# Kernel tuning notes

Measured on AMD Instinct MI355X. Metric: run time of the kernel, lower is better.

The kernel has to match this reference:

```python
import jax, jax.numpy as jnp
import numpy as np

ALPHA = 1.0          # temperature of the Bayesian DP (init kwarg alpha)
NEG = -1e9           # -inf surrogate, safe in fp32/bf16


def conv1d_same(x, w, b):
    # x: [B, T, Cin], w: [K, Cin, Cout], 'SAME' padding, stride 1
    y = jax.lax.conv_general_dilated(x, w, window_strides=(1,), padding='SAME',
                                     dimension_numbers=('NWC', 'WIO', 'NWC'))
    return y + b


def postnet(x, ws, bs):
    # Tacotron-style conv PostNet: n_conv conv1d layers with tanh (dropout=0, eval mode)
    for w, b in zip(ws, bs):
        x = jnp.tanh(conv1d_same(x, w, b))
    return x


def bayesian_dp(W, alpha):
    """Monotonic-alignment Bayesian DP (Gumbel propagation).

    W: [B, T, S] node weights on the alignment grid (T = mel time, S = text).
    Each node (t, s) has two parents: (t-1, s) [stay] and (t-1, s-1) [advance].
      mu[t,s] = W[t,s] + (1/alpha) * logsumexp(alpha*mu[t-1,s], alpha*mu[t-1,s-1])
      pi[t,s] = softmax over the two parents -> [B, T, S, 2]
    """
    B, T, S = W.shape
    m0 = W[:, 0] + jnp.where(jnp.arange(S) == 0, 0.0, NEG)   # path must start at (0,0)
    pi0 = jnp.broadcast_to(jnp.array([1.0, 0.0], W.dtype), (B, S, 2))

    def step(prev, w_t):
        # prev: [B, S] = mu[t-1]; shifted: mu[t-1, s-1]
        shifted = jnp.concatenate([jnp.full((B, 1), NEG, prev.dtype), prev[:, :-1]], axis=1)
        stacked = jnp.stack([prev, shifted], axis=-1)         # [B, S, 2]
        m = w_t + jax.nn.logsumexp(alpha * stacked, axis=-1) / alpha
        pi_t = jax.nn.softmax(alpha * stacked, axis=-1)
        return m, (m, pi_t)

    _, (ms, pis) = jax.lax.scan(step, m0, jnp.swapaxes(W, 0, 1)[1:])  # scan over T-1
    mu = jnp.concatenate([m0[:, None], jnp.swapaxes(ms, 0, 1)], axis=1)    # [B, T, S]
    pi = jnp.concatenate([pi0[:, None], jnp.swapaxes(pis, 0, 1)], axis=1)  # [B, T, S, 2]
    return mu, pi


def setup_inputs() -> dict:
    key = jax.random.key(0)
    ks = jax.random.split(key, 6)
    B, T, S = 32, 2000, 400
    NMELS, H, K = 80, 256, 5
    inputs = jax.random.normal(ks[0], (B, T, NMELS), dtype=jnp.float32)
    src_enc = jax.random.normal(ks[1], (B, S, H), dtype=jnp.float32)
    mask = jnp.ones((B, T, S), dtype=jnp.float32)
    w1 = jax.random.normal(ks[2], (K, NMELS, H), dtype=jnp.float32) * 0.05
    w2 = jax.random.normal(ks[3], (K, H, H), dtype=jnp.float32) * 0.05
    w3 = jax.random.normal(ks[4], (K, H, H), dtype=jnp.float32) * 0.05
    b1 = jnp.zeros((H,), jnp.float32)
    b2 = jnp.zeros((H,), jnp.float32)
    b3 = jnp.zeros((H,), jnp.float32)
    return {"inputs": inputs, "src_enc": src_enc, "mask": mask,
            "w1": w1, "b1": b1, "w2": w2, "b2": b2, "w3": w3, "b3": b3}


def reference(inputs, src_enc, mask, w1, b1, w2, b2, w3, b3):
    # PostNet over mel frames -> spec embeddings matching src_enc dim
    Wspec = postnet(inputs, [w1, w2, w3], [b1, b2, b3])       # [B, T, H]
    # attention score grid
    W = jnp.einsum('bth,bsh->bts', Wspec, src_enc)            # [B, T, S]
    alignments = jax.nn.softmax(W, axis=1)                    # softmax over mel-time (dim 1)
    mu, pi = bayesian_dp(alignments * mask, ALPHA)
    return mu, pi, alignments, Wspec
```

## Files before the change

kernel.cpp:

```cpp
#include <hip/hip_runtime.h>
#include <hip/hip_bf16.h>

#define B_ 32
#define T_ 2000
#define S_ 400
#define C0_ 80
#define H_ 256

static constexpr float NEGV = -1e9f;
static constexpr int NMU  = B_ * T_ * S_;
static constexpr int NPI  = 2 * NMU;

typedef _Float16 f16x8 __attribute__((ext_vector_type(8)));
typedef float    f32x4 __attribute__((ext_vector_type(4)));

__global__ __launch_bounds__(256)
void wprep(const float* __restrict__ w, _Float16* __restrict__ wcat,
           int CIN, int CPAD)
{
  const int tot = 256 * 5 * CPAD;
  int idx = blockIdx.x * 256 + threadIdx.x;
  if (idx >= tot) return;
  int co  = idx / (5 * CPAD);
  int rem = idx - co * (5 * CPAD);
  int k   = rem / CPAD;
  int ci  = rem - k * CPAD;
  float v = (ci < CIN) ? w[((size_t)k * CIN + ci) * H_ + co] : 0.f;
  wcat[idx] = (_Float16)v;
}

__global__ __launch_bounds__(256)
void ecast(const float* __restrict__ e, _Float16* __restrict__ ef)
{
  const int n4 = B_ * S_ * H_ / 4;
  int idx = blockIdx.x * 256 + threadIdx.x;
  if (idx >= n4) return;
  float4 v = ((const float4*)e)[idx];
  _Float16* d = ef + (size_t)idx * 4;
  d[0] = (_Float16)v.x; d[1] = (_Float16)v.y;
  d[2] = (_Float16)v.z; d[3] = (_Float16)v.w;
}

template<int CIN, int CPAD, bool INF32, bool OUTF32>
__global__ __launch_bounds__(256)
void conv_mfma(const void* __restrict__ xin, const _Float16* __restrict__ wcat,
               const float* __restrict__ bias, void* __restrict__ yout)
{
  constexpr int KK  = 5 * CPAD;
  constexpr int NS  = KK / 32;
  constexpr int STR = CPAD + 8;
  __shared__ _Float16 xs[68 * STR];
  const int b   = blockIdx.y;
  const int t0  = blockIdx.x * 64;
  const int tid = threadIdx.x;
  const int w   = tid >> 6;
  const int l   = tid & 63;

  if constexpr (INF32) {
    const float* xb = (const float*)xin + (size_t)b * T_ * CIN;
    constexpr int NG = CPAD / 4;
    for (int idx = tid; idx < 68 * NG; idx += 256) {
      int j = idx / NG, g = idx - j * NG;
      int t = t0 - 2 + j;
      int c = g * 4;
      float4 v = make_float4(0.f, 0.f, 0.f, 0.f);
      if (t >= 0 && t < T_ && c < CIN) v = *(const float4*)&xb[(size_t)t * CIN + c];
      _Float16* d = &xs[j * STR + c];
      d[0] = (_Float16)v.x; d[1] = (_Float16)v.y;
      d[2] = (_Float16)v.z; d[3] = (_Float16)v.w;
    }
  } else {
    const _Float16* xb = (const _Float16*)xin + (size_t)b * T_ * CIN;
    constexpr int NG = CPAD / 8;
    for (int idx = tid; idx < 68 * NG; idx += 256) {
      int j = idx / NG, g = idx - j * NG;
      int t = t0 - 2 + j;
      f16x8 v = {(_Float16)0,(_Float16)0,(_Float16)0,(_Float16)0,
                 (_Float16)0,(_Float16)0,(_Float16)0,(_Float16)0};
      if (t >= 0 && t < T_) v = *(const f16x8*)&xb[(size_t)t * CIN + g * 8];
      *(f16x8*)&xs[j * STR + g * 8] = v;
    }
  }
  __syncthreads();

  const int lr = l & 15;
  const int lk = (l >> 4) * 8;

  f32x4 acc[4][4];
  const f32x4 zz = {0.f, 0.f, 0.f, 0.f};
#pragma unroll
  for (int i = 0; i < 4; i++)
#pragma unroll
    for (int j = 0; j < 4; j++) acc[i][j] = zz;

  const _Float16* wbase = wcat + (size_t)(w * 64 + lr) * KK + lk;

  for (int kk = 0; kk < NS; kk++) {
    const int p  = kk * 32;
    const int k  = p / CPAD;
    const int ci = p - k * CPAD;
    f16x8 a0 = *(const f16x8*)&xs[( 0 + lr + k) * STR + ci + lk];
    f16x8 a1 = *(const f16x8*)&xs[(16 + lr + k) * STR + ci + lk];
    f16x8 a2 = *(const f16x8*)&xs[(32 + lr + k) * STR + ci + lk];
    f16x8 a3 = *(const f16x8*)&xs[(48 + lr + k) * STR + ci + lk];
    f16x8 w0 = *(const f16x8*)&wbase[(size_t)( 0) * KK + p];
    f16x8 w1 = *(const f16x8*)&wbase[(size_t)(16) * KK + p];
    f16x8 w2 = *(const f16x8*)&wbase[(size_t)(32) * KK + p];
    f16x8 w3 = *(const f16x8*)&wbase[(size_t)(48) * KK + p];
    acc[0][0] = __builtin_amdgcn_mfma_f32_16x16x32_f16(a0, w0, acc[0][0], 0, 0, 0);
    acc[0][1] = __builtin_amdgcn_mfma_f32_16x16x32_f16(a0, w1, acc[0][1], 0, 0, 0);
    acc[0][2] = __builtin_amdgcn_mfma_f32_16x16x32_f16(a0, w2, acc[0][2], 0, 0, 0);
    acc[0][3] = __builtin_amdgcn_mfma_f32_16x16x32_f16(a0, w3, acc[0][3], 0, 0, 0);
    acc[1][0] = __builtin_amdgcn_mfma_f32_16x16x32_f16(a1, w0, acc[1][0], 0, 0, 0);
    acc[1][1] = __builtin_amdgcn_mfma_f32_16x16x32_f16(a1, w1, acc[1][1], 0, 0, 0);
    acc[1][2] = __builtin_amdgcn_mfma_f32_16x16x32_f16(a1, w2, acc[1][2], 0, 0, 0);
    acc[1][3] = __builtin_amdgcn_mfma_f32_16x16x32_f16(a1, w3, acc[1][3], 0, 0, 0);
    acc[2][0] = __builtin_amdgcn_mfma_f32_16x16x32_f16(a2, w0, acc[2][0], 0, 0, 0);
    acc[2][1] = __builtin_amdgcn_mfma_f32_16x16x32_f16(a2, w1, acc[2][1], 0, 0, 0);
    acc[2][2] = __builtin_amdgcn_mfma_f32_16x16x32_f16(a2, w2, acc[2][2], 0, 0, 0);
    acc[2][3] = __builtin_amdgcn_mfma_f32_16x16x32_f16(a2, w3, acc[2][3], 0, 0, 0);
    acc[3][0] = __builtin_amdgcn_mfma_f32_16x16x32_f16(a3, w0, acc[3][0], 0, 0, 0);
    acc[3][1] = __builtin_amdgcn_mfma_f32_16x16x32_f16(a3, w1, acc[3][1], 0, 0, 0);
    acc[3][2] = __builtin_amdgcn_mfma_f32_16x16x32_f16(a3, w2, acc[3][2], 0, 0, 0);
    acc[3][3] = __builtin_amdgcn_mfma_f32_16x16x32_f16(a3, w3, acc[3][3], 0, 0, 0);
  }

#pragma unroll
  for (int ct = 0; ct < 4; ct++) {
    const int co = w * 64 + ct * 16 + lr;
    const float bv = bias[co];
#pragma unroll
    for (int tt = 0; tt < 4; tt++) {
#pragma unroll
      for (int r = 0; r < 4; r++) {
        const int t = t0 + tt * 16 + (l >> 4) * 4 + r;
        if (t < T_) {
          float v = tanhf(acc[tt][ct][r] + bv);
          if constexpr (OUTF32)
            ((float*)yout)[((size_t)b * T_ + t) * H_ + co] = v;
          else
            ((_Float16*)yout)[((size_t)b * T_ + t) * H_ + co] = (_Float16)v;
        }
      }
    }
  }
}

__global__ __launch_bounds__(256)
void einsum_mfma(const float* __restrict__ A, const _Float16* __restrict__ E,
                 float* __restrict__ Wg,
                 float* __restrict__ pm, float* __restrict__ pl)
{
  constexpr int STR = H_ + 8;
  __shared__ _Float16 xs[64 * STR];
  const int b   = blockIdx.z;
  const int t0  = blockIdx.x * 64;
  const int s0  = blockIdx.y * 256;
  const int tid = threadIdx.x;
  const int w   = tid >> 6;
  const int l   = tid & 63;

  const float* Ab = A + (size_t)b * T_ * H_;
  for (int idx = tid; idx < 64 * 64; idx += 256) {
    int row = idx >> 6, g = idx & 63;
    int t = t0 + row;
    float4 v = make_float4(0.f, 0.f, 0.f, 0.f);
    if (t < T_) v = *(const float4*)&Ab[(size_t)t * H_ + 4 * g];
    _Float16* d = &xs[row * STR + 4 * g];
    d[0] = (_Float16)v.x; d[1] = (_Float16)v.y;
    d[2] = (_Float16)v.z; d[3] = (_Float16)v.w;
  }
  __syncthreads();

  const int lr = l & 15;
  const int lk = (l >> 4) * 8;

  f32x4 acc[4][4];
  const f32x4 zz = {0.f, 0.f, 0.f, 0.f};
#pragma unroll
  for (int i = 0; i < 4; i++)
#pragma unroll
    for (int j = 0; j < 4; j++) acc[i][j] = zz;

  const _Float16* Eb = E + (size_t)b * S_ * H_;
  const int sr = s0 + w * 64 + lr;
  const _Float16* e0 = Eb + (size_t)((sr      < S_) ? sr      : (S_ - 1)) * H_ + lk;
  const _Float16* e1 = Eb + (size_t)((sr + 16 < S_) ? sr + 16 : (S_ - 1)) * H_ + lk;
  const _Float16* e2 = Eb + (size_t)((sr + 32 < S_) ? sr + 32 : (S_ - 1)) * H_ + lk;
  const _Float16* e3 = Eb + (size_t)((sr + 48 < S_) ? sr + 48 : (S_ - 1)) * H_ + lk;

#pragma unroll
  for (int kk = 0; kk < 8; kk++) {
    const int p = kk * 32;
    f16x8 a0 = *(const f16x8*)&xs[( 0 + lr) * STR + p + lk];
    f16x8 a1 = *(const f16x8*)&xs[(16 + lr) * STR + p + lk];
    f16x8 a2 = *(const f16x8*)&xs[(32 + lr) * STR + p + lk];
    f16x8 a3 = *(const f16x8*)&xs[(48 + lr) * STR + p + lk];
    f16x8 w0 = *(const f16x8*)&e0[p];
    f16x8 w1 = *(const f16x8*)&e1[p];
    f16x8 w2 = *(const f16x8*)&e2[p];
    f16x8 w3 = *(const f16x8*)&e3[p];
    acc[0][0] = __builtin_amdgcn_mfma_f32_16x16x32_f16(a0, w0, acc[0][0], 0, 0, 0);
    acc[0][1] = __builtin_amdgcn_mfma_f32_16x16x32_f16(a0, w1, acc[0][1], 0, 0, 0);
    acc[0][2] = __builtin_amdgcn_mfma_f32_16x16x32_f16(a0, w2, acc[0][2], 0, 0, 0);
    acc[0][3] = __builtin_amdgcn_mfma_f32_16x16x32_f16(a0, w3, acc[0][3], 0, 0, 0);
    acc[1][0] = __builtin_amdgcn_mfma_f32_16x16x32_f16(a1, w0, acc[1][0], 0, 0, 0);
    acc[1][1] = __builtin_amdgcn_mfma_f32_16x16x32_f16(a1, w1, acc[1][1], 0, 0, 0);
    acc[1][2] = __builtin_amdgcn_mfma_f32_16x16x32_f16(a1, w2, acc[1][2], 0, 0, 0);
    acc[1][3] = __builtin_amdgcn_mfma_f32_16x16x32_f16(a1, w3, acc[1][3], 0, 0, 0);
    acc[2][0] = __builtin_amdgcn_mfma_f32_16x16x32_f16(a2, w0, acc[2][0], 0, 0, 0);
    acc[2][1] = __builtin_amdgcn_mfma_f32_16x16x32_f16(a2, w1, acc[2][1], 0, 0, 0);
    acc[2][2] = __builtin_amdgcn_mfma_f32_16x16x32_f16(a2, w2, acc[2][2], 0, 0, 0);
    acc[2][3] = __builtin_amdgcn_mfma_f32_16x16x32_f16(a2, w3, acc[2][3], 0, 0, 0);
    acc[3][0] = __builtin_amdgcn_mfma_f32_16x16x32_f16(a3, w0, acc[3][0], 0, 0, 0);
    acc[3][1] = __builtin_amdgcn_mfma_f32_16x16x32_f16(a3, w1, acc[3][1], 0, 0, 0);
    acc[3][2] = __builtin_amdgcn_mfma_f32_16x16x32_f16(a3, w2, acc[3][2], 0, 0, 0);
    acc[3][3] = __builtin_amdgcn_mfma_f32_16x16x32_f16(a3, w3, acc[3][3], 0, 0, 0);
  }

  float* Wb = Wg + (size_t)b * T_ * S_;
#pragma unroll
  for (int ct = 0; ct < 4; ct++) {
    const int s = s0 + w * 64 + ct * 16 + lr;
    if (s < S_) {
#pragma unroll
      for (int tt = 0; tt < 4; tt++) {
#pragma unroll
        for (int r = 0; r < 4; r++) {
          const int t = t0 + tt * 16 + (l >> 4) * 4 + r;
          if (t < T_) Wb[(size_t)t * S_ + s] = acc[tt][ct][r];
        }
      }
    }
  }

  const int tblk = blockIdx.x;
#pragma unroll
  for (int ct = 0; ct < 4; ct++) {
    float M = -3e38f;
#pragma unroll
    for (int tt = 0; tt < 4; tt++)
#pragma unroll
      for (int r = 0; r < 4; r++) {
        const int t = t0 + tt * 16 + (l >> 4) * 4 + r;
        if (t < T_) M = fmaxf(M, acc[tt][ct][r]);
      }
    float L = 0.f;
#pragma unroll
    for (int tt = 0; tt < 4; tt++)
#pragma unroll
      for (int r = 0; r < 4; r++) {
        const int t = t0 + tt * 16 + (l >> 4) * 4 + r;
        if (t < T_) L += __expf(acc[tt][ct][r] - M);
      }
#pragma unroll
    for (int mk = 16; mk <= 32; mk <<= 1) {
      float Mo = __shfl_xor(M, mk);
      float Lo = __shfl_xor(L, mk);
      float Mn = fmaxf(M, Mo);
      L = L * __expf(M - Mn) + Lo * __expf(Mo - Mn);
      M = Mn;
    }
    if ((l >> 4) == 0) {
      const int s = s0 + w * 64 + ct * 16 + lr;
      if (s < S_) {
        pm[((size_t)b * 32 + tblk) * S_ + s] = M;
        pl[((size_t)b * 32 + tblk) * S_ + s] = L;
      }
    }
  }
}

__global__ __launch_bounds__(256)
void stats_reduce(const float* __restrict__ pm, const float* __restrict__ pl,
                  float* __restrict__ statsOut)
{
  int idx = blockIdx.x * 256 + threadIdx.x;
  if (idx >= B_ * S_) return;
  int b = idx / S_, s = idx - b * S_;
  float M = -3e38f, L = 0.f;
#pragma unroll 4
  for (int k = 0; k < 32; k++) {
    float m = pm[((size_t)b * 32 + k) * S_ + s];
    float l = pl[((size_t)b * 32 + k) * S_ + s];
    float Mn = fmaxf(M, m);
    L = L * __expf(M - Mn) + l * __expf(m - Mn);
    M = Mn;
  }
  statsOut[(size_t)b * S_ + s] = M + __logf(L);
}

__global__ __launch_bounds__(256)
void norm_kernel(float* __restrict__ al, const float* __restrict__ Mk,
                 const float* __restrict__ stats, float* __restrict__ wdp)
{
  constexpr float C2 = 1.44269504f;
  const int gid = blockIdx.x * 256 + threadIdx.x;
  if (gid >= NMU / 4) return;
  const int b   = gid / (T_ * S_ / 4);
  const int rem = gid - b * (T_ * S_ / 4);
  const int s4  = rem % (S_ / 4);
  const float4 st4 = *(const float4*)&stats[(size_t)b * S_ + 4 * s4];
  float4 r = ((const float4*)al)[gid];
  float4 k = ((const float4*)Mk)[gid];
  float4 a;
  a.x = __expf(r.x - st4.x);
  a.y = __expf(r.y - st4.y);
  a.z = __expf(r.z - st4.z);
  a.w = __expf(r.w - st4.w);
  ((float4*)al)[gid] = a;
  ((float4*)wdp)[gid] = make_float4(a.x * k.x * C2, a.y * k.y * C2,
                                    a.z * k.z * C2, a.w * k.w * C2);
}

__global__ __launch_bounds__(256, 1)
void dp_skew3(const float* Wdp, float* muOut, float* piOut)
{
  __shared__ float ring[96 * S_];
  __shared__ float bnd[64][4];
  const int b = blockIdx.x;
  const int w = threadIdx.x >> 6;
  const int l = threadIdx.x & 63;
  const int lc = (l < 50) ? l : 49;
  const bool act = (l < 50);
  const int sc = 100 * w + 2 * lc;

  const float* wb  = Wdp   + (size_t)b * T_ * S_;
  float*       mub = muOut + (size_t)b * T_ * S_;
  float*       pib = piOut + (size_t)(2 * b) * T_ * S_;

  constexpr float LN2  = 0.693147181f;
  constexpr float NEGN = -1.44269504e9f;

#define DMA(row, slot)                                                      \
  { const char* s_ = (const char*)(wb + (size_t)(row) * S_);                \
    char* d_ = (char*)ring + ((slot) * 1600);                               \
    __builtin_amdgcn_global_load_lds(                                       \
      (const __attribute__((address_space(1))) void*)(s_ + l * 16),         \
      (__attribute__((address_space(3))) void*)(d_ + l * 16), 16, 0, 0);    \
    if (l < 36)                                                             \
      __builtin_amdgcn_global_load_lds(                                     \
        (const __attribute__((address_space(1))) void*)(s_ + 1024 + l*16),  \
        (__attribute__((address_space(3))) void*)(d_ + 1024 + l*16), 16, 0, 0); }

#pragma unroll
  for (int i = 0; i < 4; ++i) { const int r0 = 4 * w + i; DMA(r0, r0) }
  if (w == 0) DMA(16, 16)
  asm volatile("s_waitcnt vmcnt(0)" ::: "memory");
  __syncthreads();

  float n0 = NEGN, n1 = NEGN;
  int rs = 1;
  int ds = 17 + 4 * w;

  for (int p = 0; p <= 128; ++p) {
    __builtin_amdgcn_s_barrier();
    asm volatile("s_waitcnt vmcnt(40)" ::: "memory");
    const int j = p - w - 1;

    {
      const int dr = 16 * (p + 1) + 1 + 4 * w;
#pragma unroll
      for (int q = 0; q < 4; ++q) {
        if (dr + q < T_) {
          int s2 = ds + q; if (s2 >= 96) s2 -= 96;
          DMA(dr + q, s2)
        }
      }
      ds += 16; if (ds >= 96) ds -= 96;
    }

    if (p == w) {
      float2 c0v = *(const float2*)&ring[sc];
      n0 = c0v.x + ((sc == 0) ? 0.f : NEGN);
      n1 = c0v.y + NEGN;
      if (act) {
        *(float2*)&mub[sc] = make_float2(n0 * LN2, n1 * LN2);
        *(float4*)&pib[2 * sc] = make_float4(1.f, 0.f, 1.f, 0.f);
      }
      if (l == 49) bnd[0][w] = n1;
    } else if (j >= 0 && j <= 124) {
      const int tb = 16 * j + 1;
      float2 cur[16];
      float  bq[16];
#pragma unroll
      for (int k = 0; k < 16; ++k) {
        const int t = tb + k;
        int sk = rs + k; if (sk >= 96) sk -= 96;
        cur[k] = (t < T_) ? *(const float2*)&ring[sk * S_ + sc]
                          : make_float2(0.f, 0.f);
        bq[k] = (w > 0) ? bnd[(t - 1) & 63][w - 1] : NEGN;
      }
      float* mrow = mub + (size_t)tb * S_ + sc;
      float* prow = pib + (size_t)tb * (2 * S_) + 2 * sc;
#pragma unroll
      for (int k = 0; k < 16; ++k) {
        const int t = tb + k;
        if (t < T_) {
          float sh = __shfl_up(n1, 1);
          float sft0 = (l == 0) ? bq[k] : sh;
          float d0 = n0 - sft0;
          float e0; asm("v_exp_f32 %0, %1" : "=v"(e0) : "v"(-fabsf(d0)));
          float q0 = 1.f + e0;
          float lg0; asm("v_log_f32 %0, %1" : "=v"(lg0) : "v"(q0));
          float rc0; asm("v_rcp_f32 %0, %1" : "=v"(rc0) : "v"(q0));
          float p00 = (d0 >= 0.f) ? rc0 : 1.f - rc0;
          float nn0 = cur[k].x + fmaxf(n0, sft0) + lg0;
          float d1 = n1 - n0;
          float e1; asm("v_exp_f32 %0, %1" : "=v"(e1) : "v"(-fabsf(d1)));
          float q1 = 1.f + e1;
          float lg1; asm("v_log_f32 %0, %1" : "=v"(lg1) : "v"(q1));
          float rc1; asm("v_rcp_f32 %0, %1" : "=v"(rc1) : "v"(q1));
          float p01 = (d1 >= 0.f) ? rc1 : 1.f - rc1;
          float nn1 = cur[k].y + fmaxf(n1, n0) + lg1;
          if (act) {
            *(float2*)mrow = make_float2(nn0 * LN2, nn1 * LN2);
            *(float4*)prow = make_float4(p00, 1.f - p00, p01, 1.f - p01);
          }
          n0 = nn0; n1 = nn1;
          if (l == 49) bnd[t & 63][w] = n1;
        }
        mrow += S_;
        prow += 2 * S_;
      }
      rs += 16; if (rs >= 96) rs -= 96;
    }
    asm volatile("s_waitcnt lgkmcnt(0)" ::: "memory");
  }
#undef DMA
}

extern "C" void kernel_launch(void* const* d_in, const int* in_sizes, int n_in,
                              void* d_out, int out_size, void* d_ws, size_t ws_size,
                              hipStream_t stream)
{
  (void)in_sizes; (void)n_in; (void)out_size; (void)d_ws; (void)ws_size;
  const float* x   = (const float*)d_in[0];
  const float* enc = (const float*)d_in[1];
  const float* msk = (const float*)d_in[2];
  const float* w1  = (const float*)d_in[3];
  const float* b1  = (const float*)d_in[4];
  const float* w2  = (const float*)d_in[5];
  const float* b2  = (const float*)d_in[6];
  const float* w3  = (const float*)d_in[7];
  const float* b3  = (const float*)d_in[8];

  float* out = (float*)d_out;
  float* mu  = out;
  float* pi  = out + NMU;
  float* al  = out + NMU + NPI;
  float* wsp = out + NMU + NPI + NMU;

  _Float16*  h1  = (_Float16*)(pi + 26000000);
  _Float16*  h2  = (_Float16*)(pi + 35000000);
  _Float16*  wc1 = (_Float16*)(pi + 44000000);
  _Float16*  wc2 = (_Float16*)(pi + 44100000);
  _Float16*  wc3 = (_Float16*)(pi + 44300000);
  _Float16*  encf = (_Float16*)(pi + 44600000);
  float*     pm   = pi + 46300000;
  float*     pl   = pi + 47200000;
  float*     pistats = pi + NPI - 13056;

  hipLaunchKernelGGL(wprep, dim3((256*5*96 +255)/256), dim3(256), 0, stream, w1, wc1, C0_, 96);
  hipLaunchKernelGGL(wprep, dim3((256*5*256+255)/256), dim3(256), 0, stream, w2, wc2, H_, 256);
  hipLaunchKernelGGL(wprep, dim3((256*5*256+255)/256), dim3(256), 0, stream, w3, wc3, H_, 256);
  hipLaunchKernelGGL(ecast, dim3(B_*S_*H_/4/256), dim3(256), 0, stream, enc, encf);

  dim3 cgrid((T_ + 63) / 64, B_);
  hipLaunchKernelGGL((conv_mfma<C0_,  96, true,  false>), cgrid, dim3(256), 0, stream,
                     (const void*)x,  wc1, b1, (void*)h1);
  hipLaunchKernelGGL((conv_mfma<H_,  256, false, false>), cgrid, dim3(256), 0, stream,
                     (const void*)h1, wc2, b2, (void*)h2);
  hipLaunchKernelGGL((conv_mfma<H_,  256, false, true >), cgrid, dim3(256), 0, stream,
                     (const void*)h2, wc3, b3, (void*)wsp);

  hipLaunchKernelGGL(einsum_mfma, dim3((T_ + 63) / 64, (S_ + 255) / 256, B_), dim3(256),
                     0, stream, wsp, encf, al, pm, pl);
  hipLaunchKernelGGL(stats_reduce, dim3((B_ * S_ + 255) / 256), dim3(256), 0, stream,
                     pm, pl, pistats);
  hipLaunchKernelGGL(norm_kernel, dim3(NMU / 4 / 256), dim3(256), 0, stream, al, msk, pistats, mu);
  hipLaunchKernelGGL(dp_skew3, dim3(B_), dim3(256), 0, stream, mu, mu, pi);
}
```

Measured before the change: 926.1 us.

## Stage DP weights in fp16 inside pi buffer and deepen LDS ring

The normalised DP weights are now written as fp16 into an unused tail region of each batch's pi slice instead of fp32 into mu. The DP kernel streams them at half the bytes, using a 144-row fp16 LDS ring and 24 timesteps per pipeline phase, which gives fewer barrier phases. The per-column stats are parked in mu's first row, to be overwritten later. This removes the DP's fp32 reread traffic and some barrier overhead. The cost is fp16 rounding of the DP inputs and tricky buffer aliasing: each batch's scratch must be consumed before later writes clobber it.

```diff
diff --git a/kernel.cpp b/kernel.cpp
--- a/kernel.cpp
+++ b/kernel.cpp
@@ -12,6 +12,8 @@
 static constexpr int NPI  = 2 * NMU;
 
 typedef _Float16 f16x8 __attribute__((ext_vector_type(8)));
+typedef _Float16 f16x4v __attribute__((ext_vector_type(4)));
+typedef _Float16 f16x2v __attribute__((ext_vector_type(2)));
 typedef float    f32x4 __attribute__((ext_vector_type(4)));
 
 __global__ __launch_bounds__(256)
@@ -273,7 +275,7 @@
 
 __global__ __launch_bounds__(256)
 void stats_reduce(const float* __restrict__ pm, const float* __restrict__ pl,
-                  float* __restrict__ statsOut)
+                  float* __restrict__ statsMu)
 {
   int idx = blockIdx.x * 256 + threadIdx.x;
   if (idx >= B_ * S_) return;
@@ -287,20 +289,21 @@
     L = L * __expf(M - Mn) + l * __expf(m - Mn);
     M = Mn;
   }
-  statsOut[(size_t)b * S_ + s] = M + __logf(L);
+  statsMu[(size_t)b * T_ * S_ + s] = M + __logf(L);
 }
 
 __global__ __launch_bounds__(256)
 void norm_kernel(float* __restrict__ al, const float* __restrict__ Mk,
-                 const float* __restrict__ stats, float* __restrict__ wdp)
+                 const float* __restrict__ statsMu, float* __restrict__ piBase)
 {
   constexpr float C2 = 1.44269504f;
   const int gid = blockIdx.x * 256 + threadIdx.x;
   if (gid >= NMU / 4) return;
   const int b   = gid / (T_ * S_ / 4);
   const int rem = gid - b * (T_ * S_ / 4);
+  const int t   = rem / (S_ / 4);
   const int s4  = rem % (S_ / 4);
-  const float4 st4 = *(const float4*)&stats[(size_t)b * S_ + 4 * s4];
+  const float4 st4 = *(const float4*)&statsMu[(size_t)b * T_ * S_ + 4 * s4];
   float4 r = ((const float4*)al)[gid];
   float4 k = ((const float4*)Mk)[gid];
   float4 a;
@@ -309,14 +312,16 @@
   a.z = __expf(r.z - st4.z);
   a.w = __expf(r.w - st4.w);
   ((float4*)al)[gid] = a;
-  ((float4*)wdp)[gid] = make_float4(a.x * k.x * C2, a.y * k.y * C2,
-                                    a.z * k.z * C2, a.w * k.w * C2);
+  _Float16* wdpf = (_Float16*)(piBase + (size_t)b * 1600000 + 1200000);
+  f16x4v h = {(_Float16)(a.x * k.x * C2), (_Float16)(a.y * k.y * C2),
+              (_Float16)(a.z * k.z * C2), (_Float16)(a.w * k.w * C2)};
+  *(f16x4v*)&wdpf[(size_t)t * S_ + 4 * s4] = h;
 }
 
 __global__ __launch_bounds__(256, 1)
-void dp_skew3(const float* Wdp, float* muOut, float* piOut)
-{
-  __shared__ float ring[96 * S_];
+void dp_skew4(float* muOut, float* piBase)
+{
+  __shared__ _Float16 ring[144 * S_];
   __shared__ float bnd[64][4];
   const int b = blockIdx.x;
   const int w = threadIdx.x >> 6;
@@ -325,76 +330,77 @@
   const bool act = (l < 50);
   const int sc = 100 * w + 2 * lc;
 
-  const float* wb  = Wdp   + (size_t)b * T_ * S_;
-  float*       mub = muOut + (size_t)b * T_ * S_;
-  float*       pib = piOut + (size_t)(2 * b) * T_ * S_;
+  const _Float16* wbf = (const _Float16*)(piBase + (size_t)b * 1600000 + 1200000);
+  float* mub = muOut + (size_t)b * T_ * S_;
+  float* pib = piBase + (size_t)(2 * b) * T_ * S_;
 
   constexpr float LN2  = 0.693147181f;
   constexpr float NEGN = -1.44269504e9f;
 
 #define DMA(row, slot)                                                      \
-  { const char* s_ = (const char*)(wb + (size_t)(row) * S_);                \
-    char* d_ = (char*)ring + ((slot) * 1600);                               \
-    __builtin_amdgcn_global_load_lds(                                       \
-      (const __attribute__((address_space(1))) void*)(s_ + l * 16),         \
-      (__attribute__((address_space(3))) void*)(d_ + l * 16), 16, 0, 0);    \
-    if (l < 36)                                                             \
+  { const char* s_ = (const char*)(wbf + (size_t)(row) * S_);               \
+    char* d_ = (char*)ring + ((slot) * 800);                                \
+    if (l < 50)                                                             \
       __builtin_amdgcn_global_load_lds(                                     \
-        (const __attribute__((address_space(1))) void*)(s_ + 1024 + l*16),  \
-        (__attribute__((address_space(3))) void*)(d_ + 1024 + l*16), 16, 0, 0); }
-
-#pragma unroll
-  for (int i = 0; i < 4; ++i) { const int r0 = 4 * w + i; DMA(r0, r0) }
-  if (w == 0) DMA(16, 16)
+        (const __attribute__((address_space(1))) void*)(s_ + l * 16),       \
+        (__attribute__((address_space(3))) void*)(d_ + l * 16), 16, 0, 0); }
+
+#pragma unroll
+  for (int i = 0; i < 6; ++i) { const int r0 = 6 * w + i; DMA(r0, r0) }
+  if (w == 0) DMA(24, 24)
   asm volatile("s_waitcnt vmcnt(0)" ::: "memory");
   __syncthreads();
 
   float n0 = NEGN, n1 = NEGN;
   int rs = 1;
-  int ds = 17 + 4 * w;
-
-  for (int p = 0; p <= 128; ++p) {
+  int ds = 25 + 6 * w;
+
+  for (int p = 0; p <= 87; ++p) {
     __builtin_amdgcn_s_barrier();
-    asm volatile("s_waitcnt vmcnt(40)" ::: "memory");
+    asm volatile("s_waitcnt vmcnt(54)" ::: "memory");
     const int j = p - w - 1;
 
     {
-      const int dr = 16 * (p + 1) + 1 + 4 * w;
-#pragma unroll
-      for (int q = 0; q < 4; ++q) {
+      const int dr = 24 * (p + 1) + 1 + 6 * w;
+#pragma unroll
+      for (int q = 0; q < 6; ++q) {
         if (dr + q < T_) {
-          int s2 = ds + q; if (s2 >= 96) s2 -= 96;
+          int s2 = ds + q; if (s2 >= 144) s2 -= 144;
           DMA(dr + q, s2)
         }
       }
-      ds += 16; if (ds >= 96) ds -= 96;
+      ds += 24; if (ds >= 144) ds -= 144;
     }
 
     if (p == w) {
-      float2 c0v = *(const float2*)&ring[sc];
-      n0 = c0v.x + ((sc == 0) ? 0.f : NEGN);
-      n1 = c0v.y + NEGN;
+      f16x2v c0h = *(const f16x2v*)&ring[sc];
+      n0 = (float)c0h[0] + ((sc == 0) ? 0.f : NEGN);
+      n1 = (float)c0h[1] + NEGN;
       if (act) {
         *(float2*)&mub[sc] = make_float2(n0 * LN2, n1 * LN2);
         *(float4*)&pib[2 * sc] = make_float4(1.f, 0.f, 1.f, 0.f);
       }
       if (l == 49) bnd[0][w] = n1;
-    } else if (j >= 0 && j <= 124) {
-      const int tb = 16 * j + 1;
-      float2 cur[16];
-      float  bq[16];
-#pragma unroll
-      for (int k = 0; k < 16; ++k) {
+    } else if (j >= 0 && j <= 83) {
+      const int tb = 24 * j + 1;
+      float2 cur[24];
+      float  bq[24];
+#pragma unroll
+      for (int k = 0; k < 24; ++k) {
         const int t = tb + k;
-        int sk = rs + k; if (sk >= 96) sk -= 96;
-        cur[k] = (t < T_) ? *(const float2*)&ring[sk * S_ + sc]
-                          : make_float2(0.f, 0.f);
+        int sk = rs + k; if (sk >= 144) sk -= 144;
+        if (t < T_) {
+          f16x2v h = *(const f16x2v*)&ring[sk * S_ + sc];
+          cur[k] = make_float2((float)h[0], (float)h[1]);
+        } else {
+          cur[k] = make_float2(0.f, 0.f);
+        }
         bq[k] = (w > 0) ? bnd[(t - 1) & 63][w - 1] : NEGN;
       }
       float* mrow = mub + (size_t)tb * S_ + sc;
       float* prow = pib + (size_t)tb * (2 * S_) + 2 * sc;
 #pragma unroll
-      for (int k = 0; k < 16; ++k) {
+      for (int k = 0; k < 24; ++k) {
         const int t = tb + k;
         if (t < T_) {
           float sh = __shfl_up(n1, 1);
@@ -423,7 +429,7 @@
         mrow += S_;
         prow += 2 * S_;
       }
-      rs += 16; if (rs >= 96) rs -= 96;
+      rs += 24; if (rs >= 144) rs -= 144;
     }
     asm volatile("s_waitcnt lgkmcnt(0)" ::: "memory");
   }
@@ -459,7 +465,6 @@
   _Float16*  encf = (_Float16*)(pi + 44600000);
   float*     pm   = pi + 46300000;
   float*     pl   = pi + 47200000;
-  float*     pistats = pi + NPI - 13056;
 
   hipLaunchKernelGGL(wprep, dim3((256*5*96 +255)/256), dim3(256), 0, stream, w1, wc1, C0_, 96);
   hipLaunchKernelGGL(wprep, dim3((256*5*256+255)/256), dim3(256), 0, stream, w2, wc2, H_, 256);
@@ -477,7 +482,7 @@
   hipLaunchKernelGGL(einsum_mfma, dim3((T_ + 63) / 64, (S_ + 255) / 256, B_), dim3(256),
                      0, stream, wsp, encf, al, pm, pl);
   hipLaunchKernelGGL(stats_reduce, dim3((B_ * S_ + 255) / 256), dim3(256), 0, stream,
-                     pm, pl, pistats);
-  hipLaunchKernelGGL(norm_kernel, dim3(NMU / 4 / 256), dim3(256), 0, stream, al, msk, pistats, mu);
-  hipLaunchKernelGGL(dp_skew3, dim3(B_), dim3(256), 0, stream, mu, mu, pi);
-}
+                     pm, pl, mu);
+  hipLaunchKernelGGL(norm_kernel, dim3(NMU / 4 / 256), dim3(256), 0, stream, al, msk, mu, pi);
+  hipLaunchKernelGGL(dp_skew4, dim3(B_), dim3(256), 0, stream, mu, pi);
+}
```

After: 941.1 us. Within noise of the previous version (+1.6%).
